# Kernel tuning notes

Measured on AMD Instinct MI355X. Metric: run time of the kernel, lower is better.

Reference implementation:

```python
import jax, jax.numpy as jnp
import numpy as np

N_ADAPTERS = 64
RANK = 64
ALPHA = 1.0
SCALING = ALPHA / RANK


def setup_inputs() -> dict:
    key = jax.random.key(0)
    k1, k2, k3, k4 = jax.random.split(key, 4)
    x = jax.random.normal(k1, (16, 2048, 4096), dtype=jnp.float32)
    adapter_ids = jax.random.randint(k2, (16,), 0, N_ADAPTERS, dtype=jnp.int64)
    # A init: randn * 0.02 (as in module). B is zeros in the module init, but we
    # use small random values so the reference exercises nontrivial math.
    A = jax.random.normal(k3, (N_ADAPTERS, 4096, RANK), dtype=jnp.float32) * 0.02
    B = jax.random.normal(k4, (N_ADAPTERS, RANK, 4096), dtype=jnp.float32) * 0.02
    return {"x": x, "adapter_ids": adapter_ids, "A": A, "B": B}


def reference(x, adapter_ids, A, B):
    # Gather per-sample low-rank factors: [b, r, in], [b, out, r]
    B_req = B[adapter_ids]
    A_req = A[adapter_ids]
    # Bx: [b, n, r]
    Bx = jnp.einsum('bni,bri->bnr', x, B_req)
    # out: [b, n, out]
    out = jnp.einsum('bnr,bor->bno', Bx, A_req)
    return out * SCALING
```

## Files before the change

### kernel.cpp

```cpp
#include <hip/hip_runtime.h>
#include <hip/hip_bf16.h>


typedef __bf16 bf16x8 __attribute__((ext_vector_type(8)));
typedef float  f32x4  __attribute__((ext_vector_type(4)));

#define N_BATCH 16
#define SEQLEN  2048
#define D_IN    4096
#define D_OUT   4096
#define RNK     64
#define TN      64
#define BK      128
#define BKP     136
#define BXP     72

__device__ __forceinline__ bf16x8 cvt8(f32x4 a, f32x4 b) {
    bf16x8 r;
    r[0] = (__bf16)a[0]; r[1] = (__bf16)a[1]; r[2] = (__bf16)a[2]; r[3] = (__bf16)a[3];
    r[4] = (__bf16)b[0]; r[5] = (__bf16)b[1]; r[6] = (__bf16)b[2]; r[7] = (__bf16)b[3];
    return r;
}

__global__ __launch_bounds__(256, 2) void lora_fused(
    const float* __restrict__ x, const int* __restrict__ ids,
    const float* __restrict__ A, const float* __restrict__ Bw,
    float* __restrict__ out)
{
    __shared__ __bf16 xs[TN * BKP];
    __shared__ __bf16 bxs[TN * BXP];

    const int tid  = threadIdx.x;
    const int wave = tid >> 6;
    const int lane = tid & 63;
    const int l15  = lane & 15;
    const int quad = lane >> 4;

    const int blk  = blockIdx.x;
    const int slot = blk >> 3;
    const int b    = (blk & 7) * 2 + (slot >> 5);
    const int nt   = slot & 31;

    const int aid = ids[b];
    const float* xb = x   + ((size_t)b * SEQLEN + (size_t)nt * TN) * D_IN;
    float*       ob = out + ((size_t)b * SEQLEN + (size_t)nt * TN) * D_OUT;
    const float* Aq = A  + (size_t)aid * D_OUT * RNK;
    const float* Bq = Bw + (size_t)aid * RNK * D_IN;

    f32x4 zero; zero[0] = zero[1] = zero[2] = zero[3] = 0.0f;

    f32x4 acc[4];
    #pragma unroll
    for (int t = 0; t < 4; ++t) acc[t] = zero;

    const int srow = tid >> 2;
    const int sq   = tid & 3;
    const float* xsrc = xb + (size_t)srow * D_IN + sq * 32;
    __bf16* xdst = &xs[srow * BKP + sq * 32];
    const float* bsrc = Bq + (size_t)(wave * 16 + l15) * D_IN + quad * 8;

    for (int kb = 0; kb < D_IN / BK; ++kb) {
        __syncthreads();
        const float* sp = xsrc + kb * BK;
        #pragma unroll
        for (int i = 0; i < 4; ++i) {
            f32x4 v0 = __builtin_nontemporal_load((const f32x4*)(sp + i * 8));
            f32x4 v1 = __builtin_nontemporal_load((const f32x4*)(sp + i * 8 + 4));
            *(bf16x8*)(xdst + i * 8) = cvt8(v0, v1);
        }
        __syncthreads();

        const float* bp = bsrc + kb * BK;
        #pragma unroll
        for (int s = 0; s < 4; ++s) {
            f32x4 b0 = *(const f32x4*)(bp + s * 32);
            f32x4 b1 = *(const f32x4*)(bp + s * 32 + 4);
            bf16x8 bfrag = cvt8(b0, b1);
            #pragma unroll
            for (int t = 0; t < 4; ++t) {
                bf16x8 afrag = *(const bf16x8*)&xs[(t * 16 + l15) * BKP + s * 32 + quad * 8];
                acc[t] = __builtin_amdgcn_mfma_f32_16x16x32_bf16(afrag, bfrag, acc[t], 0, 0, 0);
            }
        }
    }

    #pragma unroll
    for (int t = 0; t < 4; ++t)
        #pragma unroll
        for (int j = 0; j < 4; ++j)
            bxs[(t * 16 + quad * 4 + j) * BXP + wave * 16 + l15] =
                (__bf16)(acc[t][j] * 0.015625f);
    __syncthreads();

    bf16x8 a2[4][2];
    #pragma unroll
    for (int t = 0; t < 4; ++t)
        #pragma unroll
        for (int s = 0; s < 2; ++s)
            a2[t][s] = *(const bf16x8*)&bxs[(t * 16 + l15) * BXP + s * 32 + quad * 8];

    for (int oc = 0; oc < 16; ++oc) {
        const int o0 = oc * 256 + wave * 64;
        bf16x8 b2[4][2];
        #pragma unroll
        for (int ot = 0; ot < 4; ++ot) {
            const float* ap = Aq + (size_t)(o0 + ot * 16 + l15) * RNK + quad * 8;
            #pragma unroll
            for (int s = 0; s < 2; ++s) {
                f32x4 a0 = *(const f32x4*)(ap + s * 32);
                f32x4 a1 = *(const f32x4*)(ap + s * 32 + 4);
                b2[ot][s] = cvt8(a0, a1);
            }
        }
        f32x4 acc2[4][4];
        #pragma unroll
        for (int t = 0; t < 4; ++t)
            #pragma unroll
            for (int ot = 0; ot < 4; ++ot)
                acc2[t][ot] = zero;
        #pragma unroll
        for (int s = 0; s < 2; ++s)
            #pragma unroll
            for (int ot = 0; ot < 4; ++ot)
                #pragma unroll
                for (int t = 0; t < 4; ++t)
                    acc2[t][ot] = __builtin_amdgcn_mfma_f32_16x16x32_bf16(
                        a2[t][s], b2[ot][s], acc2[t][ot], 0, 0, 0);
        #pragma unroll
        for (int t = 0; t < 4; ++t)
            #pragma unroll
            for (int j = 0; j < 4; ++j)
                #pragma unroll
                for (int ot = 0; ot < 4; ++ot)
                    __builtin_nontemporal_store(
                        acc2[t][ot][j],
                        ob + (size_t)(t * 16 + quad * 4 + j) * D_OUT + o0 + ot * 16 + l15);
    }
}

extern "C" void kernel_launch(void* const* d_in, const int* in_sizes, int n_in,
                              void* d_out, int out_size, void* d_ws, size_t ws_size,
                              hipStream_t stream) {
    (void)in_sizes; (void)n_in; (void)d_ws; (void)ws_size; (void)out_size;
    const float* x   = (const float*)d_in[0];
    const int*   ids = (const int*)d_in[1];
    const float* A   = (const float*)d_in[2];
    const float* B   = (const float*)d_in[3];
    float*       out = (float*)d_out;

    dim3 grid(512), block(256);
    hipLaunchKernelGGL(lora_fused, grid, block, 0, stream, x, ids, A, B, out);
}
```

Baseline: 1.122 ms.

## Halve row tile, double-buffer x staging with register prefetch, raise occupancy

Shrinks the per-block row tile from 64 to 32, doubling the grid to 1024 blocks and raising launch bounds to 4 blocks per CU. The x tile staging is now double-buffered in LDS: the next K-slice is loaded into registers before the current slice's MFMAs run, then written to the other buffer afterwards, leaving one barrier per iteration instead of two. The output stores switch from nontemporal to plain stores. The aim is to hide global load latency on this memory-bound kernel. The cost is that B and A are re-read by twice as many blocks, and the single custom s_waitcnt/s_barrier sequence is the only guard on the double-buffer handoff.

```diff
diff --git a/kernel.cpp b/kernel.cpp
--- a/kernel.cpp
+++ b/kernel.cpp
@@ -5,13 +5,13 @@
 typedef __bf16 bf16x8 __attribute__((ext_vector_type(8)));
 typedef float  f32x4  __attribute__((ext_vector_type(4)));
 
-#define N_BATCH 16
 #define SEQLEN  2048
 #define D_IN    4096
 #define D_OUT   4096
 #define RNK     64
-#define TN      64
+#define TN      32
 #define BK      128
+#define NKB     (D_IN / BK)
 #define BKP     136
 #define BXP     72
 
@@ -22,12 +22,12 @@
     return r;
 }
 
-__global__ __launch_bounds__(256, 2) void lora_fused(
+__global__ __launch_bounds__(256, 4) void lora_fused(
     const float* __restrict__ x, const int* __restrict__ ids,
     const float* __restrict__ A, const float* __restrict__ Bw,
     float* __restrict__ out)
 {
-    __shared__ __bf16 xs[TN * BKP];
+    __shared__ __bf16 xs[2][TN * BKP];
     __shared__ __bf16 bxs[TN * BXP];
 
     const int tid  = threadIdx.x;
@@ -38,8 +38,8 @@
 
     const int blk  = blockIdx.x;
     const int slot = blk >> 3;
-    const int b    = (blk & 7) * 2 + (slot >> 5);
-    const int nt   = slot & 31;
+    const int b    = (blk & 7) * 2 + (slot >> 6);
+    const int nt   = slot & 63;
 
     const int aid = ids[b];
     const float* xb = x   + ((size_t)b * SEQLEN + (size_t)nt * TN) * D_IN;
@@ -49,52 +49,65 @@
 
     f32x4 zero; zero[0] = zero[1] = zero[2] = zero[3] = 0.0f;
 
-    f32x4 acc[4];
-    #pragma unroll
-    for (int t = 0; t < 4; ++t) acc[t] = zero;
+    f32x4 acc[2];
+    acc[0] = zero; acc[1] = zero;
 
-    const int srow = tid >> 2;
-    const int sq   = tid & 3;
-    const float* xsrc = xb + (size_t)srow * D_IN + sq * 32;
-    __bf16* xdst = &xs[srow * BKP + sq * 32];
+    const int srow = tid >> 3;
+    const int sq   = tid & 7;
+    const float* xsrc = xb + (size_t)srow * D_IN + sq * 16;
     const float* bsrc = Bq + (size_t)(wave * 16 + l15) * D_IN + quad * 8;
 
-    for (int kb = 0; kb < D_IN / BK; ++kb) {
-        __syncthreads();
-        const float* sp = xsrc + kb * BK;
+    f32x4 pre[4];
+    {
         #pragma unroll
-        for (int i = 0; i < 4; ++i) {
-            f32x4 v0 = __builtin_nontemporal_load((const f32x4*)(sp + i * 8));
-            f32x4 v1 = __builtin_nontemporal_load((const f32x4*)(sp + i * 8 + 4));
-            *(bf16x8*)(xdst + i * 8) = cvt8(v0, v1);
+        for (int i = 0; i < 4; ++i)
+            pre[i] = __builtin_nontemporal_load((const f32x4*)(xsrc + i * 4));
+        __bf16* xd = &xs[0][srow * BKP + sq * 16];
+        *(bf16x8*)xd       = cvt8(pre[0], pre[1]);
+        *(bf16x8*)(xd + 8) = cvt8(pre[2], pre[3]);
+    }
+
+    for (int kb = 0; kb < NKB; ++kb) {
+        if (kb + 1 < NKB) {
+            const float* sp = xsrc + (size_t)(kb + 1) * BK;
+            #pragma unroll
+            for (int i = 0; i < 4; ++i)
+                pre[i] = __builtin_nontemporal_load((const f32x4*)(sp + i * 4));
         }
-        __syncthreads();
+        asm volatile("s_waitcnt lgkmcnt(0)\n\ts_barrier" ::: "memory");
 
-        const float* bp = bsrc + kb * BK;
+        const float* bp = bsrc + (size_t)kb * BK;
+        const __bf16* xc = xs[kb & 1];
         #pragma unroll
         for (int s = 0; s < 4; ++s) {
             f32x4 b0 = *(const f32x4*)(bp + s * 32);
             f32x4 b1 = *(const f32x4*)(bp + s * 32 + 4);
             bf16x8 bfrag = cvt8(b0, b1);
             #pragma unroll
-            for (int t = 0; t < 4; ++t) {
-                bf16x8 afrag = *(const bf16x8*)&xs[(t * 16 + l15) * BKP + s * 32 + quad * 8];
+            for (int t = 0; t < 2; ++t) {
+                bf16x8 afrag = *(const bf16x8*)&xc[(t * 16 + l15) * BKP + s * 32 + quad * 8];
                 acc[t] = __builtin_amdgcn_mfma_f32_16x16x32_bf16(afrag, bfrag, acc[t], 0, 0, 0);
             }
+        }
+
+        if (kb + 1 < NKB) {
+            __bf16* xd = &xs[(kb + 1) & 1][srow * BKP + sq * 16];
+            *(bf16x8*)xd       = cvt8(pre[0], pre[1]);
+            *(bf16x8*)(xd + 8) = cvt8(pre[2], pre[3]);
         }
     }
 
     #pragma unroll
-    for (int t = 0; t < 4; ++t)
+    for (int t = 0; t < 2; ++t)
         #pragma unroll
         for (int j = 0; j < 4; ++j)
             bxs[(t * 16 + quad * 4 + j) * BXP + wave * 16 + l15] =
                 (__bf16)(acc[t][j] * 0.015625f);
     __syncthreads();
 
-    bf16x8 a2[4][2];
+    bf16x8 a2[2][2];
     #pragma unroll
-    for (int t = 0; t < 4; ++t)
+    for (int t = 0; t < 2; ++t)
         #pragma unroll
         for (int s = 0; s < 2; ++s)
             a2[t][s] = *(const bf16x8*)&bxs[(t * 16 + l15) * BXP + s * 32 + quad * 8];
@@ -112,9 +125,9 @@
                 b2[ot][s] = cvt8(a0, a1);
             }
         }
-        f32x4 acc2[4][4];
+        f32x4 acc2[2][4];
         #pragma unroll
-        for (int t = 0; t < 4; ++t)
+        for (int t = 0; t < 2; ++t)
             #pragma unroll
             for (int ot = 0; ot < 4; ++ot)
                 acc2[t][ot] = zero;
@@ -123,18 +136,17 @@
             #pragma unroll
             for (int ot = 0; ot < 4; ++ot)
                 #pragma unroll
-                for (int t = 0; t < 4; ++t)
+                for (int t = 0; t < 2; ++t)
                     acc2[t][ot] = __builtin_amdgcn_mfma_f32_16x16x32_bf16(
                         a2[t][s], b2[ot][s], acc2[t][ot], 0, 0, 0);
         #pragma unroll
-        for (int t = 0; t < 4; ++t)
+        for (int t = 0; t < 2; ++t)
             #pragma unroll
             for (int j = 0; j < 4; ++j)
                 #pragma unroll
                 for (int ot = 0; ot < 4; ++ot)
-                    __builtin_nontemporal_store(
-                        acc2[t][ot][j],
-                        ob + (size_t)(t * 16 + quad * 4 + j) * D_OUT + o0 + ot * 16 + l15);
+                    ob[(size_t)(t * 16 + quad * 4 + j) * D_OUT + o0 + ot * 16 + l15] =
+                        acc2[t][ot][j];
     }
 }
 
@@ -148,6 +160,6 @@
     const float* B   = (const float*)d_in[3];
     float*       out = (float*)d_out;
 
-    dim3 grid(512), block(256);
+    dim3 grid(1024), block(256);
     hipLaunchKernelGGL(lora_fused, grid, block, 0, stream, x, ids, A, B, out);
 }
```

Measured after the change: 1.092 ms. 1.03x faster.
